# Kernel optimization log

Measured on AMD Instinct MI355X. Metric: run time of the kernel, lower is better.

## Reference

```python
import jax, jax.numpy as jnp
import numpy as np

N, M, EMBED, DFF = 4, 1, 2048, 8192
INPUT_DIM = (N // M) * EMBED   # 8192
BLOCK = EMBED // M             # 2048
B = 4096
DT_MIN, DT_MAX, DT_INIT = 1e-3, 1.0, 0.01
EPS = 1.1920929e-7  # torch.finfo(float32).eps, RMSNorm default


def setup_inputs() -> dict:
    key = jax.random.key(0)
    ks = jax.random.split(key, 16)
    rn = lambda k, *s: jax.random.normal(k, s, jnp.float32)
    logit_n = float(np.log(1.0 / (N - 1)))
    t = (DT_INIT - DT_MIN) / (DT_MAX - DT_MIN)
    dt_bias = float(np.log(t / (1.0 - t)))
    return {
        "x": rn(ks[0], B, N, BLOCK),
        "read_in_p": logit_n + 0.01 * rn(ks[1], N, M),
        "write_out_p": 0.01 * rn(ks[2], N, M),
        "alpha_read_in": jnp.full((1,), 0.01, jnp.float32),
        "alpha_write_out": jnp.full((1,), 0.01, jnp.float32),
        "W_ri": 0.01 * rn(ks[3], N * M, INPUT_DIM),
        "W_wo": 0.01 * rn(ks[4], N * M, INPUT_DIM),
        "log_dt_conserv": jnp.full((1,), dt_bias, jnp.float32),
        "log_dt_diss": jnp.full((1,), dt_bias, jnp.float32),
        "W_dtc": 0.01 * rn(ks[5], 1, INPUT_DIM),
        "b_dtc": jnp.zeros((1,), jnp.float32),
        "W_dtd": 0.01 * rn(ks[6], 1, INPUT_DIM),
        "b_dtd": jnp.zeros((1,), jnp.float32),
        "conserv_A": jnp.eye(N, dtype=jnp.float32) + 0.01 * rn(ks[7], N, N),
        "W_conv": 0.01 * rn(ks[8], N * N, INPUT_DIM),
        "diss_diag": jnp.full((N,), -8.0, jnp.float32),
        "W_diss": 0.01 * rn(ks[9], N, INPUT_DIM),
        "W1": 0.02 * rn(ks[10], EMBED, DFF),
        "W2": 0.02 * rn(ks[11], DFF, EMBED),
    }


def reference(x, read_in_p, write_out_p, alpha_read_in, alpha_write_out,
              W_ri, W_wo, log_dt_conserv, log_dt_diss, W_dtc, b_dtc,
              W_dtd, b_dtd, conserv_A, W_conv, diss_diag, W_diss, W1, W2):
    Bsz = x.shape[0]
    xf = x.reshape(Bsz, INPUT_DIM)
    # RMSNorm (no affine)
    xn = xf * jax.lax.rsqrt(jnp.mean(xf * xf, axis=-1, keepdims=True) + EPS)

    # dynamic read/write weights
    h_ri = (xn @ W_ri.T).reshape(Bsz, N, M)
    h_wo = (xn @ W_wo.T).reshape(Bsz, N, M)
    read_in = jax.nn.sigmoid(alpha_read_in * h_ri + read_in_p).transpose(0, 2, 1)  # [B,M,N]
    write_out = 2.0 * jax.nn.sigmoid(alpha_write_out * h_wo + write_out_p)          # [B,N,M]

    # conservative (skew-symmetric) generator with sigmoid-gated dt
    Mmat = conserv_A + (xn @ W_conv.T).reshape(Bsz, N, N)
    skew = 0.5 * (Mmat - jnp.swapaxes(Mmat, -1, -2))
    dt_c = DT_MIN + (DT_MAX - DT_MIN) * jax.nn.sigmoid(log_dt_conserv + xn @ W_dtc.T + b_dtc)  # [B,1]
    skew = dt_c[:, :, None] * skew

    # dissipative diagonal generator
    d = jax.nn.softplus(diss_diag + xn @ W_diss.T)  # [B,N]
    dt_d = DT_MIN + (DT_MAX - DT_MIN) * jax.nn.sigmoid(log_dt_diss + xn @ W_dtd.T + b_dtd)  # [B,1]
    Dd = -dt_d * d                                   # [B,N]

    # Strang split: exp(D/2) * Cayley(S) * exp(D/2), Cayley ~ solve(I-S, I+S) in fp32
    ehD = jnp.exp(0.5 * Dd)
    I = jnp.eye(N, dtype=jnp.float32)
    exp_S = jnp.linalg.solve(I - skew.astype(jnp.float32), I + skew.astype(jnp.float32)).astype(x.dtype)
    Phi = ehD[:, :, None] * exp_S * ehD[:, None, :]  # [B,N,N]

    # wrapped module branch: read streams -> MLP -> write back
    branch = jnp.einsum('bmn,bnd->bmd', read_in, x).reshape(Bsz, EMBED)
    y = jax.nn.gelu(branch @ W1) @ W2                # [B, EMBED]
    Y = jnp.einsum('bnm,bmd->bnd', write_out, y.reshape(Bsz, M, BLOCK))

    # stream mixing (projection='none')
    return jnp.einsum('bij,bjd->bid', Phi, x) + Y
```

## Files before the change

kernel.cpp:

```cpp
#include <hip/hip_runtime.h>
#include <cstdint>

#define Bsz       4096
#define Nn        4
#define EMBED     2048
#define DFF       8192
#define INPUT_DIM 8192
#define BLOCKD    2048
#define EPSf      1.1920929e-7f

typedef short bf16x8 __attribute__((ext_vector_type(8)));
typedef float f32x4  __attribute__((ext_vector_type(4)));

typedef __attribute__((address_space(3))) void* lds_vp;
typedef __attribute__((address_space(1))) void* gbl_vp;

__device__ __forceinline__ float sigmoidf_(float v) { return 1.0f / (1.0f + expf(-v)); }
__device__ __forceinline__ float gelu_tanh(float v) {
    const float c = 0.7978845608028654f;
    float t = tanhf(c * (v + 0.044715f * v * v * v));
    return 0.5f * v * (1.0f + t);
}
__device__ __forceinline__ float dot4(float4 a, float4 b) {
    return a.x * b.x + a.y * b.y + a.z * b.z + a.w * b.w;
}
__device__ __forceinline__ unsigned short f2bf(float f) {
    union { float f; unsigned u; } c; c.f = f; return (unsigned short)(c.u >> 16);
}
__device__ __forceinline__ float bf2f(unsigned short h) {
    union { float f; unsigned u; } c; c.u = ((unsigned)h) << 16; return c.f;
}

__device__ __forceinline__ void gload16(const void* g, void* l) {
    __builtin_amdgcn_global_load_lds((gbl_vp)(void*)g, (lds_vp)l, 16, 0, 0);
}

__global__ __launch_bounds__(256) void rowstats_kernel(
    const float* __restrict__ x,
    const float* __restrict__ read_in_p, const float* __restrict__ write_out_p,
    const float* __restrict__ alpha_ri, const float* __restrict__ alpha_wo,
    const float* __restrict__ W_ri, const float* __restrict__ W_wo,
    const float* __restrict__ log_dt_c, const float* __restrict__ log_dt_d,
    const float* __restrict__ W_dtc, const float* __restrict__ b_dtc,
    const float* __restrict__ W_dtd, const float* __restrict__ b_dtd,
    const float* __restrict__ conserv_A, const float* __restrict__ W_conv,
    const float* __restrict__ diss_diag, const float* __restrict__ W_diss,
    float* __restrict__ phi_out, float* __restrict__ ri_out, float* __restrict__ wo_out)
{
    const int b0  = blockIdx.x * 4;
    const int tid = threadIdx.x;

    float acc[4][31];
#pragma unroll
    for (int r = 0; r < 4; ++r)
#pragma unroll
        for (int j = 0; j < 31; ++j) acc[r][j] = 0.0f;

#pragma unroll 1
    for (int i = 0; i < 8; ++i) {
        const int e = i * 1024 + tid * 4;
        float4 xv[4];
#pragma unroll
        for (int r = 0; r < 4; ++r) {
            xv[r] = *(const float4*)(x + (size_t)(b0 + r) * INPUT_DIM + e);
            acc[r][0] += dot4(xv[r], xv[r]);
        }
#pragma unroll
        for (int w = 0; w < 4; ++w) {
            const float4 wv = *(const float4*)(W_ri + (size_t)w * INPUT_DIM + e);
#pragma unroll
            for (int r = 0; r < 4; ++r) acc[r][1 + w] += dot4(xv[r], wv);
        }
#pragma unroll
        for (int w = 0; w < 4; ++w) {
            const float4 wv = *(const float4*)(W_wo + (size_t)w * INPUT_DIM + e);
#pragma unroll
            for (int r = 0; r < 4; ++r) acc[r][5 + w] += dot4(xv[r], wv);
        }
#pragma unroll
        for (int w = 0; w < 16; ++w) {
            const float4 wv = *(const float4*)(W_conv + (size_t)w * INPUT_DIM + e);
#pragma unroll
            for (int r = 0; r < 4; ++r) acc[r][9 + w] += dot4(xv[r], wv);
        }
        {
            const float4 wv = *(const float4*)(W_dtc + e);
#pragma unroll
            for (int r = 0; r < 4; ++r) acc[r][25] += dot4(xv[r], wv);
        }
        {
            const float4 wv = *(const float4*)(W_dtd + e);
#pragma unroll
            for (int r = 0; r < 4; ++r) acc[r][26] += dot4(xv[r], wv);
        }
#pragma unroll
        for (int w = 0; w < 4; ++w) {
            const float4 wv = *(const float4*)(W_diss + (size_t)w * INPUT_DIM + e);
#pragma unroll
            for (int r = 0; r < 4; ++r) acc[r][27 + w] += dot4(xv[r], wv);
        }
    }

#pragma unroll
    for (int r = 0; r < 4; ++r)
#pragma unroll
        for (int j = 0; j < 31; ++j) {
            float v = acc[r][j];
#pragma unroll
            for (int o = 32; o > 0; o >>= 1) v += __shfl_down(v, o, 64);
            acc[r][j] = v;
        }
    __shared__ float red[4][4][31];
    const int wave = tid >> 6, lane = tid & 63;
    if (lane == 0) {
#pragma unroll
        for (int r = 0; r < 4; ++r)
#pragma unroll
            for (int j = 0; j < 31; ++j) red[wave][r][j] = acc[r][j];
    }
    __syncthreads();

    if (tid < 4) {
        const int r = tid;
        const int b = b0 + r;
        float s31[31];
#pragma unroll
        for (int j = 0; j < 31; ++j)
            s31[j] = red[0][r][j] + red[1][r][j] + red[2][r][j] + red[3][r][j];

        const float s = 1.0f / sqrtf(s31[0] * (1.0f / (float)INPUT_DIM) + EPSf);

        const float a_ri = alpha_ri[0], a_wo = alpha_wo[0];
        float ri[Nn], wo[Nn];
#pragma unroll
        for (int n = 0; n < Nn; ++n) {
            ri[n] = sigmoidf_(a_ri * (s * s31[1 + n]) + read_in_p[n]);
            wo[n] = 2.0f * sigmoidf_(a_wo * (s * s31[5 + n]) + write_out_p[n]);
        }

        const float dt_c = 1e-3f + (1.0f - 1e-3f) * sigmoidf_(log_dt_c[0] + s * s31[25] + b_dtc[0]);
        const float dt_d = 1e-3f + (1.0f - 1e-3f) * sigmoidf_(log_dt_d[0] + s * s31[26] + b_dtd[0]);

        float Mmat[Nn][Nn];
#pragma unroll
        for (int i = 0; i < Nn; ++i)
#pragma unroll
            for (int j = 0; j < Nn; ++j)
                Mmat[i][j] = conserv_A[i * Nn + j] + s * s31[9 + i * Nn + j];

        float S[Nn][Nn];
#pragma unroll
        for (int i = 0; i < Nn; ++i)
#pragma unroll
            for (int j = 0; j < Nn; ++j)
                S[i][j] = dt_c * 0.5f * (Mmat[i][j] - Mmat[j][i]);

        float ehD[Nn];
#pragma unroll
        for (int n = 0; n < Nn; ++n) {
            const float v = diss_diag[n] + s * s31[27 + n];
            const float sp = (v > 20.0f) ? v : log1pf(expf(v));
            ehD[n] = expf(-0.5f * dt_d * sp);
        }

        float Am[Nn][Nn], X[Nn][Nn];
#pragma unroll
        for (int i = 0; i < Nn; ++i)
#pragma unroll
            for (int j = 0; j < Nn; ++j) {
                const float id = (i == j) ? 1.0f : 0.0f;
                Am[i][j] = id - S[i][j];
                X[i][j]  = id + S[i][j];
            }
#pragma unroll
        for (int c = 0; c < Nn; ++c) {
            const float inv = 1.0f / Am[c][c];
#pragma unroll
            for (int j = 0; j < Nn; ++j) { Am[c][j] *= inv; X[c][j] *= inv; }
#pragma unroll
            for (int rr = 0; rr < Nn; ++rr) {
                if (rr == c) continue;
                const float f = Am[rr][c];
#pragma unroll
                for (int j = 0; j < Nn; ++j) { Am[rr][j] -= f * Am[c][j]; X[rr][j] -= f * X[c][j]; }
            }
        }

        float* __restrict__ P = phi_out + (size_t)b * 16;
#pragma unroll
        for (int i = 0; i < Nn; ++i)
#pragma unroll
            for (int j = 0; j < Nn; ++j)
                P[i * Nn + j] = ehD[i] * X[i][j] * ehD[j];
#pragma unroll
        for (int n = 0; n < Nn; ++n) {
            ri_out[(size_t)b * Nn + n] = ri[n];
            wo_out[(size_t)b * Nn + n] = wo[n];
        }
    }
}

__global__ __launch_bounds__(256) void branch_kernel(
    const float* __restrict__ x, const float* __restrict__ ri,
    unsigned short* __restrict__ bh, unsigned short* __restrict__ bl)
{
    const int g = blockIdx.x * 256 + threadIdx.x;
    const int b = g >> 9;
    const int d = (g & 511) << 2;
    const float* __restrict__ xb = x + (size_t)b * INPUT_DIM;
    const float* __restrict__ r  = ri + (size_t)b * Nn;
    float4 o = make_float4(0.f, 0.f, 0.f, 0.f);
#pragma unroll
    for (int n = 0; n < Nn; ++n) {
        const float4 xv = *(const float4*)(xb + n * BLOCKD + d);
        const float rn = r[n];
        o.x = fmaf(rn, xv.x, o.x);
        o.y = fmaf(rn, xv.y, o.y);
        o.z = fmaf(rn, xv.z, o.z);
        o.w = fmaf(rn, xv.w, o.w);
    }
    ushort4 h4, l4;
    h4.x = f2bf(o.x); l4.x = f2bf(o.x - bf2f(h4.x));
    h4.y = f2bf(o.y); l4.y = f2bf(o.y - bf2f(h4.y));
    h4.z = f2bf(o.z); l4.z = f2bf(o.z - bf2f(h4.z));
    h4.w = f2bf(o.w); l4.w = f2bf(o.w - bf2f(h4.w));
    *(ushort4*)(bh + (size_t)b * EMBED + d) = h4;
    *(ushort4*)(bl + (size_t)b * EMBED + d) = l4;
}

__global__ __launch_bounds__(256) void tconv_kernel(
    const float* __restrict__ in,
    unsigned short* __restrict__ oh, unsigned short* __restrict__ ol,
    int R, int C)
{
    __shared__ float t[32][33];
    const int c0 = blockIdx.x * 32;
    const int r0 = blockIdx.y * 32;
    const int tr  = threadIdx.x >> 3;
    const int tc4 = (threadIdx.x & 7) * 4;
    const float4 v = *(const float4*)(in + (size_t)(r0 + tr) * C + c0 + tc4);
    t[tr][tc4 + 0] = v.x;
    t[tr][tc4 + 1] = v.y;
    t[tr][tc4 + 2] = v.z;
    t[tr][tc4 + 3] = v.w;
    __syncthreads();
    ushort4 h4, l4;
    {
        const float f0 = t[tc4 + 0][tr], f1 = t[tc4 + 1][tr];
        const float f2 = t[tc4 + 2][tr], f3 = t[tc4 + 3][tr];
        h4.x = f2bf(f0); l4.x = f2bf(f0 - bf2f(h4.x));
        h4.y = f2bf(f1); l4.y = f2bf(f1 - bf2f(h4.y));
        h4.z = f2bf(f2); l4.z = f2bf(f2 - bf2f(h4.z));
        h4.w = f2bf(f3); l4.w = f2bf(f3 - bf2f(h4.w));
    }
    const size_t ob = (size_t)(c0 + tr) * R + r0 + tc4;
    *(ushort4*)(oh + ob) = h4;
    *(ushort4*)(ol + ob) = l4;
}

template <int K, bool GELU>
__global__ __launch_bounds__(256) void gemm_bf16x3_kernel(
    const unsigned short* __restrict__ Ah, const unsigned short* __restrict__ Al,
    const unsigned short* __restrict__ Bh, const unsigned short* __restrict__ Bl,
    float* __restrict__ Cf,
    unsigned short* __restrict__ Ch, unsigned short* __restrict__ Cl,
    int N)
{
    constexpr int KSTEPS = K / 32;
    constexpr int TSTEPS = 3 * KSTEPS;
    __shared__ alignas(16) unsigned short smem[16384];

    const int tid = threadIdx.x;
    const int l   = tid & 63;
    const int w   = tid >> 6;
    const int wr  = w >> 1, wc = w & 1;

    const int nwg = gridDim.x * gridDim.y;
    int lin = blockIdx.y * gridDim.x + blockIdx.x;
    lin = (lin & 7) * (nwg >> 3) + (lin >> 3);
    const int bx = lin % gridDim.x;
    const int by = lin / gridDim.x;
    const int row0 = by * 128;
    const int col0 = bx * 128;

    const int srow = l >> 2;
    const int skq  = (l & 3) * 8;

    f32x4 acc[4][4];
    const f32x4 z4 = {0.f, 0.f, 0.f, 0.f};
#pragma unroll
    for (int m = 0; m < 4; ++m)
#pragma unroll
        for (int n = 0; n < 4; ++n) acc[m][n] = z4;

    auto stage = [&](int t, int buf) {
        const int s  = t / KSTEPS;
        const int kk = (t - s * KSTEPS) * 32;
        const unsigned short* Ap = (s == 2) ? Al : Ah;
        const unsigned short* Bp = (s == 1) ? Bl : Bh;
        unsigned short* base = smem + buf * 8192;
#pragma unroll
        for (int i = 0; i < 2; ++i) {
            const int c = 2 * w + i;
            gload16(Ap + (size_t)(row0 + c * 16 + srow) * K + kk + skq,
                    base + c * 512);
            gload16(Bp + (size_t)(col0 + c * 16 + srow) * K + kk + skq,
                    base + 4096 + c * 512);
        }
    };

    stage(0, 0);
    int cur = 0;
    const int kg8 = (l >> 4) * 8;
    const int fr  = l & 15;
    for (int t = 0; t < TSTEPS; ++t) {
        __syncthreads();
        if (t + 1 < TSTEPS) stage(t + 1, cur ^ 1);

        const unsigned short* As = smem + cur * 8192;
        const unsigned short* Bs = smem + cur * 8192 + 4096;
        bf16x8 a[4], b[4];
#pragma unroll
        for (int m = 0; m < 4; ++m)
            a[m] = *(const bf16x8*)(As + (wr * 64 + m * 16 + fr) * 32 + kg8);
#pragma unroll
        for (int n = 0; n < 4; ++n)
            b[n] = *(const bf16x8*)(Bs + (wc * 64 + n * 16 + fr) * 32 + kg8);
#pragma unroll
        for (int m = 0; m < 4; ++m)
#pragma unroll
            for (int n = 0; n < 4; ++n)
                acc[m][n] = __builtin_amdgcn_mfma_f32_16x16x32_bf16(a[m], b[n], acc[m][n], 0, 0, 0);
        cur ^= 1;
    }

#pragma unroll
    for (int m = 0; m < 4; ++m) {
        const int gr0 = row0 + wr * 64 + m * 16 + (l >> 4) * 4;
#pragma unroll
        for (int j = 0; j < 4; ++j) {
            const size_t rb = (size_t)(gr0 + j) * N;
#pragma unroll
            for (int n = 0; n < 4; ++n) {
                const int gc = col0 + wc * 64 + n * 16 + fr;
                float v = acc[m][n][j];
                if (GELU) {
                    v = gelu_tanh(v);
                    const unsigned short h = f2bf(v);
                    Ch[rb + gc] = h;
                    Cl[rb + gc] = f2bf(v - bf2f(h));
                } else {
                    Cf[rb + gc] = v;
                }
            }
        }
    }
}

__global__ __launch_bounds__(256) void output_kernel(
    const float* __restrict__ x, const float* __restrict__ phi,
    const float* __restrict__ wo, const float* __restrict__ y,
    float* __restrict__ out)
{
    const int g = blockIdx.x * 256 + threadIdx.x;
    const int b = g >> 9;
    const int d = (g & 511) << 2;
    const float* __restrict__ xb = x + (size_t)b * INPUT_DIM;
    float4 xj[Nn];
#pragma unroll
    for (int j = 0; j < Nn; ++j) xj[j] = *(const float4*)(xb + j * BLOCKD + d);
    const float4 yv = *(const float4*)(y + (size_t)b * EMBED + d);
    const float* __restrict__ P = phi + (size_t)b * 16;
    const float* __restrict__ wv = wo + (size_t)b * Nn;
    float* __restrict__ ob = out + (size_t)b * INPUT_DIM;
#pragma unroll
    for (int i = 0; i < Nn; ++i) {
        const float wi = wv[i];
        float4 o;
        o.x = wi * yv.x; o.y = wi * yv.y; o.z = wi * yv.z; o.w = wi * yv.w;
#pragma unroll
        for (int j = 0; j < Nn; ++j) {
            const float p = P[i * Nn + j];
            o.x = fmaf(p, xj[j].x, o.x);
            o.y = fmaf(p, xj[j].y, o.y);
            o.z = fmaf(p, xj[j].z, o.z);
            o.w = fmaf(p, xj[j].w, o.w);
        }
        *(float4*)(ob + i * BLOCKD + d) = o;
    }
}

extern "C" void kernel_launch(void* const* d_in, const int* in_sizes, int n_in,
                              void* d_out, int out_size, void* d_ws, size_t ws_size,
                              hipStream_t stream)
{
    const float* x          = (const float*)d_in[0];
    const float* read_in_p  = (const float*)d_in[1];
    const float* write_out_p= (const float*)d_in[2];
    const float* alpha_ri   = (const float*)d_in[3];
    const float* alpha_wo   = (const float*)d_in[4];
    const float* W_ri       = (const float*)d_in[5];
    const float* W_wo       = (const float*)d_in[6];
    const float* log_dt_c   = (const float*)d_in[7];
    const float* log_dt_d   = (const float*)d_in[8];
    const float* W_dtc      = (const float*)d_in[9];
    const float* b_dtc      = (const float*)d_in[10];
    const float* W_dtd      = (const float*)d_in[11];
    const float* b_dtd      = (const float*)d_in[12];
    const float* conserv_A  = (const float*)d_in[13];
    const float* W_conv     = (const float*)d_in[14];
    const float* diss_diag  = (const float*)d_in[15];
    const float* W_diss     = (const float*)d_in[16];
    const float* W1         = (const float*)d_in[17];
    const float* W2         = (const float*)d_in[18];

    char* p = (char*)d_ws;
    auto alloc = [&](size_t bytes) { char* r = p; p += (bytes + 255) & ~(size_t)255; return r; };
    float*          phi = (float*)alloc((size_t)Bsz * 16 * 4);
    float*          ri  = (float*)alloc((size_t)Bsz * Nn * 4);
    float*          wo  = (float*)alloc((size_t)Bsz * Nn * 4);
    unsigned short* bh  = (unsigned short*)alloc((size_t)Bsz * EMBED * 2);
    unsigned short* bl  = (unsigned short*)alloc((size_t)Bsz * EMBED * 2);
    unsigned short* W1h = (unsigned short*)alloc((size_t)DFF * EMBED * 2);
    unsigned short* W1l = (unsigned short*)alloc((size_t)DFF * EMBED * 2);
    unsigned short* W2h = (unsigned short*)alloc((size_t)EMBED * DFF * 2);
    unsigned short* W2l = (unsigned short*)alloc((size_t)EMBED * DFF * 2);
    unsigned short* hh  = (unsigned short*)alloc((size_t)Bsz * DFF * 2);
    unsigned short* hl  = (unsigned short*)alloc((size_t)Bsz * DFF * 2);
    float*          y   = (float*)alloc((size_t)Bsz * EMBED * 4);
    float*          outp = (float*)d_out;

    rowstats_kernel<<<Bsz / 4, 256, 0, stream>>>(
        x, read_in_p, write_out_p, alpha_ri, alpha_wo, W_ri, W_wo,
        log_dt_c, log_dt_d, W_dtc, b_dtc, W_dtd, b_dtd,
        conserv_A, W_conv, diss_diag, W_diss, phi, ri, wo);

    tconv_kernel<<<dim3(DFF / 32, EMBED / 32), 256, 0, stream>>>(W1, W1h, W1l, EMBED, DFF);
    tconv_kernel<<<dim3(EMBED / 32, DFF / 32), 256, 0, stream>>>(W2, W2h, W2l, DFF, EMBED);

    branch_kernel<<<(Bsz * 512) / 256, 256, 0, stream>>>(x, ri, bh, bl);

    gemm_bf16x3_kernel<EMBED, true><<<dim3(DFF / 128, Bsz / 128), 256, 0, stream>>>(
        bh, bl, W1h, W1l, nullptr, hh, hl, DFF);

    gemm_bf16x3_kernel<DFF, false><<<dim3(EMBED / 128, Bsz / 128), 256, 0, stream>>>(
        hh, hl, W2h, W2l, y, nullptr, nullptr, EMBED);

    output_kernel<<<(Bsz * 512) / 256, 256, 0, stream>>>(x, phi, wo, y, outp);
}
```

Measured before the change: 1.759 ms.

## Interleave hi/lo bf16x3 passes per K-step and swizzle LDS to avoid bank conflicts

The bf16x3 GEMM previously ran three separate sweeps over K (hi*hi, hi*lo, lo*hi) and reloaded A-high and B-high tiles for each sweep. It now walks K once, staging hi and lo tiles into the two LDS buffers in turn and keeping the hi fragments in registers so they serve all three products. This cuts global and LDS traffic by about a third. It also adds an XOR swizzle on the k-quad offset for both the global-to-LDS writes and the fragment reads to reduce LDS bank conflicts. The cost is more live registers and less prefetch distance, since each stage overlaps only half a K-step.

```diff
diff --git a/kernel.cpp b/kernel.cpp
--- a/kernel.cpp
+++ b/kernel.cpp
@@ -267,7 +267,6 @@
     int N)
 {
     constexpr int KSTEPS = K / 32;
-    constexpr int TSTEPS = 3 * KSTEPS;
     __shared__ alignas(16) unsigned short smem[16384];
 
     const int tid = threadIdx.x;
@@ -283,8 +282,17 @@
     const int row0 = by * 128;
     const int col0 = bx * 128;
 
-    const int srow = l >> 2;
-    const int skq  = (l & 3) * 8;
+    const int srow   = l >> 2;
+    const int skq_sw = (((l & 3) ^ ((l >> 2) & 3)) << 3);
+    const size_t aoff0 = (size_t)(row0 + (2 * w) * 16 + srow) * K + skq_sw;
+    const size_t aoff1 = aoff0 + 16 * (size_t)K;
+    const size_t boff0 = (size_t)(col0 + (2 * w) * 16 + srow) * K + skq_sw;
+    const size_t boff1 = boff0 + 16 * (size_t)K;
+    unsigned short* const ldsA = smem + (2 * w) * 512;
+    unsigned short* const ldsB = smem + 4096 + (2 * w) * 512;
+
+    const int fr    = l & 15;
+    const int kg_sw = (((l >> 4) ^ (l & 3)) << 3);
 
     f32x4 acc[4][4];
     const f32x4 z4 = {0.f, 0.f, 0.f, 0.f};
@@ -293,45 +301,52 @@
 #pragma unroll
         for (int n = 0; n < 4; ++n) acc[m][n] = z4;
 
-    auto stage = [&](int t, int buf) {
-        const int s  = t / KSTEPS;
-        const int kk = (t - s * KSTEPS) * 32;
-        const unsigned short* Ap = (s == 2) ? Al : Ah;
-        const unsigned short* Bp = (s == 1) ? Bl : Bh;
-        unsigned short* base = smem + buf * 8192;
-#pragma unroll
-        for (int i = 0; i < 2; ++i) {
-            const int c = 2 * w + i;
-            gload16(Ap + (size_t)(row0 + c * 16 + srow) * K + kk + skq,
-                    base + c * 512);
-            gload16(Bp + (size_t)(col0 + c * 16 + srow) * K + kk + skq,
-                    base + 4096 + c * 512);
-        }
+    auto stage = [&](const unsigned short* Ap, const unsigned short* Bp,
+                     size_t koff, int bufsel) {
+        const int bo = bufsel * 8192;
+        gload16(Ap + aoff0 + koff, ldsA + bo);
+        gload16(Ap + aoff1 + koff, ldsA + bo + 512);
+        gload16(Bp + boff0 + koff, ldsB + bo);
+        gload16(Bp + boff1 + koff, ldsB + bo + 512);
     };
 
-    stage(0, 0);
-    int cur = 0;
-    const int kg8 = (l >> 4) * 8;
-    const int fr  = l & 15;
-    for (int t = 0; t < TSTEPS; ++t) {
+    stage(Ah, Bh, 0, 0);
+    size_t koff = 0;
+    for (int kk = 0; kk < KSTEPS; ++kk) {
         __syncthreads();
-        if (t + 1 < TSTEPS) stage(t + 1, cur ^ 1);
-
-        const unsigned short* As = smem + cur * 8192;
-        const unsigned short* Bs = smem + cur * 8192 + 4096;
-        bf16x8 a[4], b[4];
+        stage(Al, Bl, koff, 1);
+
+        bf16x8 ah[4], bh[4];
 #pragma unroll
         for (int m = 0; m < 4; ++m)
-            a[m] = *(const bf16x8*)(As + (wr * 64 + m * 16 + fr) * 32 + kg8);
+            ah[m] = *(const bf16x8*)(smem + (wr * 64 + m * 16 + fr) * 32 + kg_sw);
 #pragma unroll
         for (int n = 0; n < 4; ++n)
-            b[n] = *(const bf16x8*)(Bs + (wc * 64 + n * 16 + fr) * 32 + kg8);
+            bh[n] = *(const bf16x8*)(smem + 4096 + (wc * 64 + n * 16 + fr) * 32 + kg_sw);
 #pragma unroll
         for (int m = 0; m < 4; ++m)
 #pragma unroll
             for (int n = 0; n < 4; ++n)
-                acc[m][n] = __builtin_amdgcn_mfma_f32_16x16x32_bf16(a[m], b[n], acc[m][n], 0, 0, 0);
-        cur ^= 1;
+                acc[m][n] = __builtin_amdgcn_mfma_f32_16x16x32_bf16(ah[m], bh[n], acc[m][n], 0, 0, 0);
+
+        __syncthreads();
+        if (kk + 1 < KSTEPS) stage(Ah, Bh, koff + 32, 0);
+
+        bf16x8 al[4], bl[4];
+#pragma unroll
+        for (int m = 0; m < 4; ++m)
+            al[m] = *(const bf16x8*)(smem + 8192 + (wr * 64 + m * 16 + fr) * 32 + kg_sw);
+#pragma unroll
+        for (int n = 0; n < 4; ++n)
+            bl[n] = *(const bf16x8*)(smem + 12288 + (wc * 64 + n * 16 + fr) * 32 + kg_sw);
+#pragma unroll
+        for (int m = 0; m < 4; ++m)
+#pragma unroll
+            for (int n = 0; n < 4; ++n) {
+                acc[m][n] = __builtin_amdgcn_mfma_f32_16x16x32_bf16(ah[m], bl[n], acc[m][n], 0, 0, 0);
+                acc[m][n] = __builtin_amdgcn_mfma_f32_16x16x32_bf16(al[m], bh[n], acc[m][n], 0, 0, 0);
+            }
+        koff += 32;
     }
 
 #pragma unroll
```

Result: faster. 1.437 ms (-18.3%).
